# Kernel tuning notes

Measured on AMD Instinct MI355X. Metric: run time of the kernel, lower is better.

Reference implementation:

```python
import jax, jax.numpy as jnp
import numpy as np

B, S, L, H = 64, 256, 4, 1024
S_DIM = 16
LN_EPS = 1e-5
BN_EPS = 1e-5
SM_EPS = 1e-15


def setup_inputs() -> dict:
    key = jax.random.key(0)
    ks = jax.random.split(key, 12)
    inp = {
        'a': jax.random.normal(ks[0], (B, S, L, H), dtype=jnp.float32),
        'b': jax.random.normal(ks[1], (B, S, L, H), dtype=jnp.float32),
        'p': jax.random.normal(ks[2], (B, L, H), dtype=jnp.float32),
        'ap': jax.random.normal(ks[3], (B,), dtype=jnp.float32),
        'bp': jax.random.normal(ks[4], (B,), dtype=jnp.float32),
        # per-layer ffnn: Linear(5H -> S_DIM), stacked over the 4 sim layers
        'ffnn_w': jax.random.normal(ks[5], (L, 5 * H, S_DIM), dtype=jnp.float32) * np.sqrt(2.0 / (5 * H)).astype(np.float32),
        'ffnn_b': jnp.zeros((L, S_DIM), dtype=jnp.float32),
        # BatchNorm1d(S_DIM*L) in eval mode
        'bn_gamma': jnp.ones((S_DIM * L,), dtype=jnp.float32),
        'bn_beta': jnp.zeros((S_DIM * L,), dtype=jnp.float32),
        'bn_rm': jnp.zeros((S_DIM * L,), dtype=jnp.float32),
        'bn_rv': jnp.ones((S_DIM * L,), dtype=jnp.float32),
        # mention_score: Linear(S_DIM*L + 2 -> 3)
        'ms_w': jax.random.normal(ks[6], (S_DIM * L + 2, 3), dtype=jnp.float32) * 0.1,
        'ms_b': jnp.zeros((3,), dtype=jnp.float32),
        # dist_ecoding: Linear(1 -> 1)
        'dist_w': jax.random.normal(ks[7], (), dtype=jnp.float32),
        'dist_b': jnp.zeros((), dtype=jnp.float32),
    }
    return inp


def _layernorm(x):
    m = x.mean(-1, keepdims=True)
    v = jnp.mean((x - m) ** 2, axis=-1, keepdims=True)
    return (x - m) / jnp.sqrt(v + LN_EPS)


def _get_mask(t):
    # 1 up to (exclusive) the first seq position whose [Layer,Feat] slice is all zero
    nonzero = jnp.logical_not(jnp.all(t == 0, axis=(2, 3))).astype(t.dtype)  # [B,S]
    return jnp.cumprod(nonzero, axis=1)


def reference(a, b, p, ap, bp, ffnn_w, ffnn_b, bn_gamma, bn_beta, bn_rm, bn_rv, ms_w, ms_b, dist_w, dist_b):
    rescale = jnp.float32(1.0 / np.sqrt(H))
    a_mask = _get_mask(a)  # [B,S]
    b_mask = _get_mask(b)

    a_ln = _layernorm(a)  # [B,S,L,H]
    b_ln = _layernorm(b)

    # attention scores per layer: [B,L,S]
    sa = jnp.einsum('bslh,blh->bls', a_ln, p) * rescale
    sb = jnp.einsum('bslh,blh->bls', b_ln, p) * rescale

    # masked softmax exactly as in the original (exp * mask / (sum + eps))
    ea = jnp.exp(sa) * a_mask[:, None, :]
    eb = jnp.exp(sb) * b_mask[:, None, :]
    attn_a = ea / (ea.sum(2, keepdims=True) + SM_EPS)
    attn_b = eb / (eb.sum(2, keepdims=True) + SM_EPS)

    pa = jnp.einsum('bls,bslh->blh', attn_a, a_ln)  # pooled a  [B,L,H]
    pb = jnp.einsum('bls,bslh->blh', attn_b, b_ln)

    feat = jnp.concatenate([p, pa, pb, p * pa, p * pb], axis=-1)  # [B,L,5H]
    y = jnp.einsum('blf,lfo->blo', feat, ffnn_w) + ffnn_b  # [B,L,S_DIM]
    y = y.reshape(y.shape[0], -1)  # concat over layers -> [B, L*S_DIM]

    # BatchNorm1d (eval) + ReLU (dropout is identity at inference)
    y = (y - bn_rm) / jnp.sqrt(bn_rv + BN_EPS) * bn_gamma + bn_beta
    y = jax.nn.relu(y)

    ape = jnp.tanh(ap[:, None] * dist_w + dist_b)  # [B,1]
    bpe = jnp.tanh(bp[:, None] * dist_w + dist_b)

    z = jnp.concatenate([y, ape, bpe], axis=1)  # [B, L*S_DIM + 2]
    return z @ ms_w + ms_b  # [B,3]
```

## Files before the change

kernel.cpp:

```cpp
#include <hip/hip_runtime.h>
#include <cstdint>
#include <cstddef>

#define BB_ 64
#define SS_ 256
#define LL_ 4
#define HH_ 1024

#define ZF_OFF   ((size_t)0)
#define MASK_OFF ((size_t)131072)
#define PA_OFF   ((size_t)163840)
#define DEN_OFF  ((size_t)1212416)
#define Y_OFF    ((size_t)1214464)
#define FZ_OFF   ((size_t)1218560)

template <int MODE>
__global__ __launch_bounds__(512) void attn_pool(const float* __restrict__ A_,
                                                 const float* __restrict__ B_,
                                                 const float* __restrict__ P_,
                                                 float* __restrict__ ws) {
  int idx = blockIdx.x;
  int shalf = idx & 1;
  int l = (idx >> 1) & 3;
  int bb = (idx >> 3) & 63;
  int t = idx >> 9;

  if (MODE == 1) {
    const int* fz = reinterpret_cast<const int*>(ws + FZ_OFF);
    if (fz[t * 64 + bb] >= SS_) return;
  }

  const float* __restrict__ X = t ? B_ : A_;
  int tid = threadIdx.x;
  int wid = tid >> 6;
  int ln = tid & 63;

  float pv[16];
  {
    const float4* pr = reinterpret_cast<const float4*>(P_ + ((size_t)bb * LL_ + l) * HH_);
#pragma unroll
    for (int k = 0; k < 4; ++k) {
      float4 v = pr[k * 64 + ln];
      pv[4 * k + 0] = v.x; pv[4 * k + 1] = v.y;
      pv[4 * k + 2] = v.z; pv[4 * k + 3] = v.w;
    }
  }

  float acc[16];
#pragma unroll
  for (int j = 0; j < 16; ++j) acc[j] = 0.f;
  float den = 0.f;

  float* zf = ws + ZF_OFF + (((size_t)t * 64 + bb) * 4 + l) * SS_;
  const float* mk = ws + MASK_OFF + ((size_t)t * 64 + bb) * SS_;

  const float* base = X + (((size_t)bb * SS_ + (size_t)shalf * 128) * LL_ + l) * HH_;

  for (int i = 0; i < 16; ++i) {
    int s_local = i * 8 + wid;
    const float4* row = reinterpret_cast<const float4*>(base + (size_t)s_local * (LL_ * HH_));
    float x[16];
    float s1 = 0.f, s2 = 0.f;
#pragma unroll
    for (int k = 0; k < 4; ++k) {
      float4 v = row[k * 64 + ln];
      x[4 * k + 0] = v.x; x[4 * k + 1] = v.y;
      x[4 * k + 2] = v.z; x[4 * k + 3] = v.w;
      s1 += v.x + v.y + v.z + v.w;
      s2 += v.x * v.x + v.y * v.y + v.z * v.z + v.w * v.w;
    }
#pragma unroll
    for (int off = 32; off > 0; off >>= 1) {
      s1 += __shfl_xor(s1, off);
      s2 += __shfl_xor(s2, off);
    }
    float m = s1 * (1.0f / 1024.0f);
    float var = s2 * (1.0f / 1024.0f) - m * m;
    float rstd = rsqrtf(var + 1e-5f);

    float d = 0.f;
#pragma unroll
    for (int j = 0; j < 16; ++j) {
      x[j] -= m;
      d += x[j] * pv[j];
    }
#pragma unroll
    for (int off = 32; off > 0; off >>= 1) d += __shfl_xor(d, off);

    float e = expf(d * rstd * 0.03125f);
    if (MODE == 0) {
      if (ln == 0) zf[shalf * 128 + s_local] = (s2 == 0.f) ? 1.f : 0.f;
    } else {
      e *= mk[shalf * 128 + s_local];
    }
    float coef = e * rstd;
#pragma unroll
    for (int j = 0; j < 16; ++j) acc[j] += coef * x[j];
    den += e;
  }

  __shared__ float sm[8 * 1024];
#pragma unroll
  for (int k = 0; k < 4; ++k) {
#pragma unroll
    for (int j = 0; j < 4; ++j) sm[wid * 1024 + (k * 64 + ln) * 4 + j] = acc[4 * k + j];
  }
  __syncthreads();
  float* pa = ws + PA_OFF + ((((size_t)shalf * 2 + t) * 64 + bb) * 4 + l) * HH_;
  for (int e2 = tid; e2 < 1024; e2 += 512) {
    float tot = 0.f;
#pragma unroll
    for (int w = 0; w < 8; ++w) tot += sm[w * 1024 + e2];
    pa[e2] = tot;
  }
  __syncthreads();
  if (ln == 0) sm[wid] = den;
  __syncthreads();
  if (tid == 0) {
    float dd = 0.f;
#pragma unroll
    for (int w = 0; w < 8; ++w) dd += sm[w];
    ws[DEN_OFF + (((size_t)shalf * 2 + t) * 64 + bb) * 4 + l] = dd;
  }
}

__global__ __launch_bounds__(256) void mask_kernel(float* __restrict__ ws) {
  int idx = blockIdx.x;
  int t = idx >> 6, bb = idx & 63;
  int s = threadIdx.x;
  const float* zf = ws + ZF_OFF + (((size_t)t * 64 + bb) * 4) * SS_;
  float z0 = zf[0 * SS_ + s], z1 = zf[1 * SS_ + s];
  float z2 = zf[2 * SS_ + s], z3 = zf[3 * SS_ + s];
  bool allzero = (z0 != 0.f) && (z1 != 0.f) && (z2 != 0.f) && (z3 != 0.f);
  int fz = allzero ? s : SS_;
#pragma unroll
  for (int off = 32; off > 0; off >>= 1) fz = min(fz, __shfl_xor(fz, off));
  __shared__ int red[4];
  int wid = s >> 6, ln = s & 63;
  if (ln == 0) red[wid] = fz;
  __syncthreads();
  int fzmin = min(min(red[0], red[1]), min(red[2], red[3]));
  ws[MASK_OFF + ((size_t)t * 64 + bb) * SS_ + s] = (s < fzmin) ? 1.f : 0.f;
  if (s == 0) reinterpret_cast<int*>(ws + FZ_OFF)[t * 64 + bb] = fzmin;
}

__global__ __launch_bounds__(256) void head_kernel(const float* __restrict__ p,
                                                   const float* __restrict__ fw,
                                                   const float* __restrict__ fb,
                                                   float* __restrict__ ws) {
  int blk = blockIdx.x;
  int bb = blk >> 2, l = blk & 3;
  int t = threadIdx.x;

  const float* den = ws + DEN_OFF;
  float inv_a = 1.0f / (den[((0 * 2 + 0) * 64 + bb) * 4 + l] +
                        den[((1 * 2 + 0) * 64 + bb) * 4 + l] + 1e-15f);
  float inv_b = 1.0f / (den[((0 * 2 + 1) * 64 + bb) * 4 + l] +
                        den[((1 * 2 + 1) * 64 + bb) * 4 + l] + 1e-15f);

  const float4* pa00 = reinterpret_cast<const float4*>(ws + PA_OFF + (((size_t)(0 * 2 + 0) * 64 + bb) * 4 + l) * HH_);
  const float4* pa10 = reinterpret_cast<const float4*>(ws + PA_OFF + (((size_t)(1 * 2 + 0) * 64 + bb) * 4 + l) * HH_);
  const float4* pb01 = reinterpret_cast<const float4*>(ws + PA_OFF + (((size_t)(0 * 2 + 1) * 64 + bb) * 4 + l) * HH_);
  const float4* pb11 = reinterpret_cast<const float4*>(ws + PA_OFF + (((size_t)(1 * 2 + 1) * 64 + bb) * 4 + l) * HH_);

  float4 pv = reinterpret_cast<const float4*>(p + ((size_t)bb * LL_ + l) * HH_)[t];
  float4 A0 = pa00[t], A1 = pa10[t], B0 = pb01[t], B1 = pb11[t];
  float av[4] = {(A0.x + A1.x) * inv_a, (A0.y + A1.y) * inv_a,
                 (A0.z + A1.z) * inv_a, (A0.w + A1.w) * inv_a};
  float bv[4] = {(B0.x + B1.x) * inv_b, (B0.y + B1.y) * inv_b,
                 (B0.z + B1.z) * inv_b, (B0.w + B1.w) * inv_b};
  float cp[4] = {pv.x, pv.y, pv.z, pv.w};

  float part[16];
#pragma unroll
  for (int o = 0; o < 16; ++o) part[o] = 0.f;

  const float* wl = fw + (size_t)l * 5120 * 16;
#pragma unroll
  for (int j = 0; j < 4; ++j) {
    int h = t * 4 + j;
    float c[5] = {cp[j], av[j], bv[j], cp[j] * av[j], cp[j] * bv[j]};
#pragma unroll
    for (int sec = 0; sec < 5; ++sec) {
      const float4* wr = reinterpret_cast<const float4*>(wl + ((size_t)sec * 1024 + h) * 16);
#pragma unroll
      for (int o4 = 0; o4 < 4; ++o4) {
        float4 w4 = wr[o4];
        part[o4 * 4 + 0] += c[sec] * w4.x;
        part[o4 * 4 + 1] += c[sec] * w4.y;
        part[o4 * 4 + 2] += c[sec] * w4.z;
        part[o4 * 4 + 3] += c[sec] * w4.w;
      }
    }
  }

  __shared__ float red[256 * 17 + 16 * 17];
#pragma unroll
  for (int o = 0; o < 16; ++o) red[t * 17 + o] = part[o];
  __syncthreads();
  {
    int o = t & 15, g = t >> 4;
    float sacc = 0.f;
#pragma unroll
    for (int i = 0; i < 16; ++i) sacc += red[(g * 16 + i) * 17 + o];
    red[256 * 17 + g * 17 + o] = sacc;
  }
  __syncthreads();
  if (t < 16) {
    float sacc = 0.f;
#pragma unroll
    for (int g = 0; g < 16; ++g) sacc += red[256 * 17 + g * 17 + t];
    ws[Y_OFF + (size_t)bb * 64 + l * 16 + t] = sacc + fb[l * 16 + t];
  }
}

__global__ __launch_bounds__(64) void out_kernel(
    const float* __restrict__ ap, const float* __restrict__ bp,
    const float* __restrict__ gam, const float* __restrict__ bet,
    const float* __restrict__ rm, const float* __restrict__ rv,
    const float* __restrict__ msw, const float* __restrict__ msb,
    const float* __restrict__ dw, const float* __restrict__ db,
    const float* __restrict__ ws, float* __restrict__ out) {
  int bb = blockIdx.x;
  int k = threadIdx.x;
  float yv = ws[Y_OFF + (size_t)bb * 64 + k];
  yv = (yv - rm[k]) * rsqrtf(rv[k] + 1e-5f) * gam[k] + bet[k];
  yv = fmaxf(yv, 0.f);
  float w0 = dw[0], b0 = db[0];
  float ape = tanhf(ap[bb] * w0 + b0);
  float bpe = tanhf(bp[bb] * w0 + b0);
#pragma unroll
  for (int c = 0; c < 3; ++c) {
    float v = yv * msw[k * 3 + c];
#pragma unroll
    for (int off = 32; off > 0; off >>= 1) v += __shfl_xor(v, off);
    if (k == 0) out[bb * 3 + c] = v + ape * msw[64 * 3 + c] + bpe * msw[65 * 3 + c] + msb[c];
  }
}

extern "C" void kernel_launch(void* const* d_in, const int* in_sizes, int n_in,
                              void* d_out, int out_size, void* d_ws, size_t ws_size,
                              hipStream_t stream) {
  (void)in_sizes; (void)n_in; (void)out_size; (void)ws_size;
  const float* a = (const float*)d_in[0];
  const float* b = (const float*)d_in[1];
  const float* p = (const float*)d_in[2];
  const float* ap = (const float*)d_in[3];
  const float* bp = (const float*)d_in[4];
  const float* ffnn_w = (const float*)d_in[5];
  const float* ffnn_b = (const float*)d_in[6];
  const float* bn_g = (const float*)d_in[7];
  const float* bn_b = (const float*)d_in[8];
  const float* bn_rm = (const float*)d_in[9];
  const float* bn_rv = (const float*)d_in[10];
  const float* ms_w = (const float*)d_in[11];
  const float* ms_b = (const float*)d_in[12];
  const float* dist_w = (const float*)d_in[13];
  const float* dist_b = (const float*)d_in[14];
  float* ws = (float*)d_ws;
  float* out = (float*)d_out;

  hipLaunchKernelGGL((attn_pool<0>), dim3(1024), dim3(512), 0, stream, a, b, p, ws);
  hipLaunchKernelGGL(mask_kernel, dim3(128), dim3(256), 0, stream, ws);
  hipLaunchKernelGGL((attn_pool<1>), dim3(1024), dim3(512), 0, stream, a, b, p, ws);
  hipLaunchKernelGGL(head_kernel, dim3(256), dim3(256), 0, stream, p, ffnn_w, ffnn_b, ws);
  hipLaunchKernelGGL(out_kernel, dim3(64), dim3(64), 0, stream,
                     ap, bp, bn_g, bn_b, bn_rm, bn_rv, ms_w, ms_b, dist_w, dist_b, ws, out);
}
```

Before: 129.0 us.

## Fuse mask and head kernels, algebraically fold mean into dot, double-buffer row loads

Folds the mask computation into the second attention pass by having each block recompute the first-zero index from the zero flags, removing a kernel launch and the mask buffer. The score dot product is computed on raw values and corrected by mean times sum(p), and the mean subtraction in the pooled accumulator is deferred to a single correction term. Row loads are software-pipelined two pairs ahead, and p is staged in shared memory. Head and output kernels are merged into one 64-block kernel that loops over layers, which cuts launches but reduces head parallelism from 256 blocks to 64.

```diff
diff --git a/kernel.cpp b/kernel.cpp
--- a/kernel.cpp
+++ b/kernel.cpp
@@ -2,104 +2,168 @@
 #include <cstdint>
 #include <cstddef>
 
-#define BB_ 64
 #define SS_ 256
 #define LL_ 4
 #define HH_ 1024
 
 #define ZF_OFF   ((size_t)0)
-#define MASK_OFF ((size_t)131072)
-#define PA_OFF   ((size_t)163840)
-#define DEN_OFF  ((size_t)1212416)
-#define Y_OFF    ((size_t)1214464)
-#define FZ_OFF   ((size_t)1218560)
+#define PA_OFF   ((size_t)131072)
+#define DEN_OFF  ((size_t)(131072 + 1048576))
 
 template <int MODE>
-__global__ __launch_bounds__(512) void attn_pool(const float* __restrict__ A_,
-                                                 const float* __restrict__ B_,
-                                                 const float* __restrict__ P_,
-                                                 float* __restrict__ ws) {
+__global__ __launch_bounds__(512, 4) void attn_pool(const float* __restrict__ A_,
+                                                    const float* __restrict__ B_,
+                                                    const float* __restrict__ P_,
+                                                    float* __restrict__ ws) {
   int idx = blockIdx.x;
   int shalf = idx & 1;
   int l = (idx >> 1) & 3;
   int bb = (idx >> 3) & 63;
   int t = idx >> 9;
-
-  if (MODE == 1) {
-    const int* fz = reinterpret_cast<const int*>(ws + FZ_OFF);
-    if (fz[t * 64 + bb] >= SS_) return;
-  }
-
-  const float* __restrict__ X = t ? B_ : A_;
   int tid = threadIdx.x;
   int wid = tid >> 6;
   int ln = tid & 63;
 
-  float pv[16];
+  __shared__ float pshare[1024];
+  __shared__ float sm[8 * 1024];
+  __shared__ int wmin[8];
+
+  int fz = SS_;
+  if (MODE == 1) {
+    int myfz = SS_;
+    if (tid < SS_) {
+      const float* zfb = ws + ZF_OFF + ((size_t)t * 64 + bb) * 4 * SS_;
+      bool az = (zfb[0 * SS_ + tid] != 0.f) && (zfb[1 * SS_ + tid] != 0.f) &&
+                (zfb[2 * SS_ + tid] != 0.f) && (zfb[3 * SS_ + tid] != 0.f);
+      myfz = az ? tid : SS_;
+    }
+#pragma unroll
+    for (int off = 32; off > 0; off >>= 1) myfz = min(myfz, __shfl_xor(myfz, off));
+    if (ln == 0) wmin[wid] = myfz;
+    __syncthreads();
+#pragma unroll
+    for (int w = 0; w < 8; ++w) fz = min(fz, wmin[w]);
+    if (fz >= SS_) return;
+    __syncthreads();
+  }
+
+  const float* __restrict__ X = t ? B_ : A_;
+
+  if (tid < 256) {
+    reinterpret_cast<float4*>(pshare)[tid] =
+        reinterpret_cast<const float4*>(P_ + ((size_t)bb * LL_ + l) * HH_)[tid];
+  }
+  __syncthreads();
+
+  float sump = 0.f;
   {
-    const float4* pr = reinterpret_cast<const float4*>(P_ + ((size_t)bb * LL_ + l) * HH_);
+    const float4 pw0 = *reinterpret_cast<const float4*>(&pshare[(0 * 64 + ln) * 4]);
+    const float4 pw1 = *reinterpret_cast<const float4*>(&pshare[(1 * 64 + ln) * 4]);
+    const float4 pw2 = *reinterpret_cast<const float4*>(&pshare[(2 * 64 + ln) * 4]);
+    const float4 pw3 = *reinterpret_cast<const float4*>(&pshare[(3 * 64 + ln) * 4]);
+    sump = (pw0.x + pw0.y + pw0.z + pw0.w) + (pw1.x + pw1.y + pw1.z + pw1.w) +
+           (pw2.x + pw2.y + pw2.z + pw2.w) + (pw3.x + pw3.y + pw3.z + pw3.w);
+#pragma unroll
+    for (int off = 32; off > 0; off >>= 1) sump += __shfl_xor(sump, off);
+  }
+
+  const float* base = X + (((size_t)bb * SS_ + (size_t)shalf * 128) * LL_ + l) * HH_;
+  float* zfp = ws + ZF_OFF + (((size_t)t * 64 + bb) * 4 + l) * SS_;
+
+  float acc[16];
+#pragma unroll
+  for (int j = 0; j < 16; ++j) acc[j] = 0.f;
+  float den = 0.f, cm = 0.f;
+
+  auto loadRow = [&](float (&dst)[16], int sl) {
+    const float4* rp = reinterpret_cast<const float4*>(base + (size_t)sl * (LL_ * HH_));
+    float4 v0 = rp[ln], v1 = rp[64 + ln], v2 = rp[128 + ln], v3 = rp[192 + ln];
+    dst[0] = v0.x;  dst[1] = v0.y;  dst[2] = v0.z;  dst[3] = v0.w;
+    dst[4] = v1.x;  dst[5] = v1.y;  dst[6] = v1.z;  dst[7] = v1.w;
+    dst[8] = v2.x;  dst[9] = v2.y;  dst[10] = v2.z; dst[11] = v2.w;
+    dst[12] = v3.x; dst[13] = v3.y; dst[14] = v3.z; dst[15] = v3.w;
+  };
+
+  auto processPair = [&](const float (&u)[16], const float (&v)[16], int slu, int slv) {
+    float a1 = 0.f, a2 = 0.f, a3 = 0.f, b1 = 0.f, b2 = 0.f, b3 = 0.f;
 #pragma unroll
     for (int k = 0; k < 4; ++k) {
-      float4 v = pr[k * 64 + ln];
-      pv[4 * k + 0] = v.x; pv[4 * k + 1] = v.y;
-      pv[4 * k + 2] = v.z; pv[4 * k + 3] = v.w;
-    }
-  }
-
-  float acc[16];
-#pragma unroll
-  for (int j = 0; j < 16; ++j) acc[j] = 0.f;
-  float den = 0.f;
-
-  float* zf = ws + ZF_OFF + (((size_t)t * 64 + bb) * 4 + l) * SS_;
-  const float* mk = ws + MASK_OFF + ((size_t)t * 64 + bb) * SS_;
-
-  const float* base = X + (((size_t)bb * SS_ + (size_t)shalf * 128) * LL_ + l) * HH_;
-
-  for (int i = 0; i < 16; ++i) {
-    int s_local = i * 8 + wid;
-    const float4* row = reinterpret_cast<const float4*>(base + (size_t)s_local * (LL_ * HH_));
-    float x[16];
-    float s1 = 0.f, s2 = 0.f;
-#pragma unroll
-    for (int k = 0; k < 4; ++k) {
-      float4 v = row[k * 64 + ln];
-      x[4 * k + 0] = v.x; x[4 * k + 1] = v.y;
-      x[4 * k + 2] = v.z; x[4 * k + 3] = v.w;
-      s1 += v.x + v.y + v.z + v.w;
-      s2 += v.x * v.x + v.y * v.y + v.z * v.z + v.w * v.w;
+      const float4 pw = *reinterpret_cast<const float4*>(&pshare[(k * 64 + ln) * 4]);
+      a1 += u[4 * k + 0] + u[4 * k + 1] + u[4 * k + 2] + u[4 * k + 3];
+      a2 = fmaf(u[4 * k + 0], u[4 * k + 0], fmaf(u[4 * k + 1], u[4 * k + 1],
+           fmaf(u[4 * k + 2], u[4 * k + 2], fmaf(u[4 * k + 3], u[4 * k + 3], a2))));
+      a3 = fmaf(u[4 * k + 0], pw.x, fmaf(u[4 * k + 1], pw.y,
+           fmaf(u[4 * k + 2], pw.z, fmaf(u[4 * k + 3], pw.w, a3))));
+      b1 += v[4 * k + 0] + v[4 * k + 1] + v[4 * k + 2] + v[4 * k + 3];
+      b2 = fmaf(v[4 * k + 0], v[4 * k + 0], fmaf(v[4 * k + 1], v[4 * k + 1],
+           fmaf(v[4 * k + 2], v[4 * k + 2], fmaf(v[4 * k + 3], v[4 * k + 3], b2))));
+      b3 = fmaf(v[4 * k + 0], pw.x, fmaf(v[4 * k + 1], pw.y,
+           fmaf(v[4 * k + 2], pw.z, fmaf(v[4 * k + 3], pw.w, b3))));
     }
 #pragma unroll
     for (int off = 32; off > 0; off >>= 1) {
-      s1 += __shfl_xor(s1, off);
-      s2 += __shfl_xor(s2, off);
-    }
-    float m = s1 * (1.0f / 1024.0f);
-    float var = s2 * (1.0f / 1024.0f) - m * m;
-    float rstd = rsqrtf(var + 1e-5f);
-
-    float d = 0.f;
-#pragma unroll
-    for (int j = 0; j < 16; ++j) {
-      x[j] -= m;
-      d += x[j] * pv[j];
-    }
-#pragma unroll
-    for (int off = 32; off > 0; off >>= 1) d += __shfl_xor(d, off);
-
-    float e = expf(d * rstd * 0.03125f);
-    if (MODE == 0) {
-      if (ln == 0) zf[shalf * 128 + s_local] = (s2 == 0.f) ? 1.f : 0.f;
-    } else {
-      e *= mk[shalf * 128 + s_local];
-    }
-    float coef = e * rstd;
-#pragma unroll
-    for (int j = 0; j < 16; ++j) acc[j] += coef * x[j];
-    den += e;
-  }
-
-  __shared__ float sm[8 * 1024];
+      a1 += __shfl_xor(a1, off); a2 += __shfl_xor(a2, off); a3 += __shfl_xor(a3, off);
+      b1 += __shfl_xor(b1, off); b2 += __shfl_xor(b2, off); b3 += __shfl_xor(b3, off);
+    }
+    {
+      float m_ = a1 * (1.f / 1024.f);
+      float var_ = fmaf(-m_, m_, a2 * (1.f / 1024.f));
+      float rstd_ = rsqrtf(var_ + 1e-5f);
+      float d_ = (a3 - m_ * sump) * rstd_ * 0.03125f;
+      float e_ = expf(d_);
+      int sg_ = shalf * 128 + slu;
+      if (MODE == 0) {
+        if (ln == 0) zfp[sg_] = (a2 == 0.f) ? 1.f : 0.f;
+      } else {
+        if (sg_ >= fz) e_ = 0.f;
+      }
+      float coef_ = e_ * rstd_;
+#pragma unroll
+      for (int j = 0; j < 16; ++j) acc[j] = fmaf(coef_, u[j], acc[j]);
+      cm = fmaf(coef_, m_, cm);
+      den += e_;
+    }
+    {
+      float m_ = b1 * (1.f / 1024.f);
+      float var_ = fmaf(-m_, m_, b2 * (1.f / 1024.f));
+      float rstd_ = rsqrtf(var_ + 1e-5f);
+      float d_ = (b3 - m_ * sump) * rstd_ * 0.03125f;
+      float e_ = expf(d_);
+      int sg_ = shalf * 128 + slv;
+      if (MODE == 0) {
+        if (ln == 0) zfp[sg_] = (b2 == 0.f) ? 1.f : 0.f;
+      } else {
+        if (sg_ >= fz) e_ = 0.f;
+      }
+      float coef_ = e_ * rstd_;
+#pragma unroll
+      for (int j = 0; j < 16; ++j) acc[j] = fmaf(coef_, v[j], acc[j]);
+      cm = fmaf(coef_, m_, cm);
+      den += e_;
+    }
+  };
+
+  float xa[16], xb[16], ya[16], yb[16];
+  loadRow(xa, wid + 0);   loadRow(xb, wid + 8);
+  loadRow(ya, wid + 16);  loadRow(yb, wid + 24);
+  processPair(xa, xb, wid + 0, wid + 8);
+  loadRow(xa, wid + 32);  loadRow(xb, wid + 40);
+  processPair(ya, yb, wid + 16, wid + 24);
+  loadRow(ya, wid + 48);  loadRow(yb, wid + 56);
+  processPair(xa, xb, wid + 32, wid + 40);
+  loadRow(xa, wid + 64);  loadRow(xb, wid + 72);
+  processPair(ya, yb, wid + 48, wid + 56);
+  loadRow(ya, wid + 80);  loadRow(yb, wid + 88);
+  processPair(xa, xb, wid + 64, wid + 72);
+  loadRow(xa, wid + 96);  loadRow(xb, wid + 104);
+  processPair(ya, yb, wid + 80, wid + 88);
+  loadRow(ya, wid + 112); loadRow(yb, wid + 120);
+  processPair(xa, xb, wid + 96, wid + 104);
+  processPair(ya, yb, wid + 112, wid + 120);
+
+#pragma unroll
+  for (int j = 0; j < 16; ++j) acc[j] -= cm;
+
 #pragma unroll
   for (int k = 0; k < 4; ++k) {
 #pragma unroll
@@ -124,97 +188,8 @@
   }
 }
 
-__global__ __launch_bounds__(256) void mask_kernel(float* __restrict__ ws) {
-  int idx = blockIdx.x;
-  int t = idx >> 6, bb = idx & 63;
-  int s = threadIdx.x;
-  const float* zf = ws + ZF_OFF + (((size_t)t * 64 + bb) * 4) * SS_;
-  float z0 = zf[0 * SS_ + s], z1 = zf[1 * SS_ + s];
-  float z2 = zf[2 * SS_ + s], z3 = zf[3 * SS_ + s];
-  bool allzero = (z0 != 0.f) && (z1 != 0.f) && (z2 != 0.f) && (z3 != 0.f);
-  int fz = allzero ? s : SS_;
-#pragma unroll
-  for (int off = 32; off > 0; off >>= 1) fz = min(fz, __shfl_xor(fz, off));
-  __shared__ int red[4];
-  int wid = s >> 6, ln = s & 63;
-  if (ln == 0) red[wid] = fz;
-  __syncthreads();
-  int fzmin = min(min(red[0], red[1]), min(red[2], red[3]));
-  ws[MASK_OFF + ((size_t)t * 64 + bb) * SS_ + s] = (s < fzmin) ? 1.f : 0.f;
-  if (s == 0) reinterpret_cast<int*>(ws + FZ_OFF)[t * 64 + bb] = fzmin;
-}
-
-__global__ __launch_bounds__(256) void head_kernel(const float* __restrict__ p,
-                                                   const float* __restrict__ fw,
-                                                   const float* __restrict__ fb,
-                                                   float* __restrict__ ws) {
-  int blk = blockIdx.x;
-  int bb = blk >> 2, l = blk & 3;
-  int t = threadIdx.x;
-
-  const float* den = ws + DEN_OFF;
-  float inv_a = 1.0f / (den[((0 * 2 + 0) * 64 + bb) * 4 + l] +
-                        den[((1 * 2 + 0) * 64 + bb) * 4 + l] + 1e-15f);
-  float inv_b = 1.0f / (den[((0 * 2 + 1) * 64 + bb) * 4 + l] +
-                        den[((1 * 2 + 1) * 64 + bb) * 4 + l] + 1e-15f);
-
-  const float4* pa00 = reinterpret_cast<const float4*>(ws + PA_OFF + (((size_t)(0 * 2 + 0) * 64 + bb) * 4 + l) * HH_);
-  const float4* pa10 = reinterpret_cast<const float4*>(ws + PA_OFF + (((size_t)(1 * 2 + 0) * 64 + bb) * 4 + l) * HH_);
-  const float4* pb01 = reinterpret_cast<const float4*>(ws + PA_OFF + (((size_t)(0 * 2 + 1) * 64 + bb) * 4 + l) * HH_);
-  const float4* pb11 = reinterpret_cast<const float4*>(ws + PA_OFF + (((size_t)(1 * 2 + 1) * 64 + bb) * 4 + l) * HH_);
-
-  float4 pv = reinterpret_cast<const float4*>(p + ((size_t)bb * LL_ + l) * HH_)[t];
-  float4 A0 = pa00[t], A1 = pa10[t], B0 = pb01[t], B1 = pb11[t];
-  float av[4] = {(A0.x + A1.x) * inv_a, (A0.y + A1.y) * inv_a,
-                 (A0.z + A1.z) * inv_a, (A0.w + A1.w) * inv_a};
-  float bv[4] = {(B0.x + B1.x) * inv_b, (B0.y + B1.y) * inv_b,
-                 (B0.z + B1.z) * inv_b, (B0.w + B1.w) * inv_b};
-  float cp[4] = {pv.x, pv.y, pv.z, pv.w};
-
-  float part[16];
-#pragma unroll
-  for (int o = 0; o < 16; ++o) part[o] = 0.f;
-
-  const float* wl = fw + (size_t)l * 5120 * 16;
-#pragma unroll
-  for (int j = 0; j < 4; ++j) {
-    int h = t * 4 + j;
-    float c[5] = {cp[j], av[j], bv[j], cp[j] * av[j], cp[j] * bv[j]};
-#pragma unroll
-    for (int sec = 0; sec < 5; ++sec) {
-      const float4* wr = reinterpret_cast<const float4*>(wl + ((size_t)sec * 1024 + h) * 16);
-#pragma unroll
-      for (int o4 = 0; o4 < 4; ++o4) {
-        float4 w4 = wr[o4];
-        part[o4 * 4 + 0] += c[sec] * w4.x;
-        part[o4 * 4 + 1] += c[sec] * w4.y;
-        part[o4 * 4 + 2] += c[sec] * w4.z;
-        part[o4 * 4 + 3] += c[sec] * w4.w;
-      }
-    }
-  }
-
-  __shared__ float red[256 * 17 + 16 * 17];
-#pragma unroll
-  for (int o = 0; o < 16; ++o) red[t * 17 + o] = part[o];
-  __syncthreads();
-  {
-    int o = t & 15, g = t >> 4;
-    float sacc = 0.f;
-#pragma unroll
-    for (int i = 0; i < 16; ++i) sacc += red[(g * 16 + i) * 17 + o];
-    red[256 * 17 + g * 17 + o] = sacc;
-  }
-  __syncthreads();
-  if (t < 16) {
-    float sacc = 0.f;
-#pragma unroll
-    for (int g = 0; g < 16; ++g) sacc += red[256 * 17 + g * 17 + t];
-    ws[Y_OFF + (size_t)bb * 64 + l * 16 + t] = sacc + fb[l * 16 + t];
-  }
-}
-
-__global__ __launch_bounds__(64) void out_kernel(
+__global__ __launch_bounds__(256) void headout_kernel(
+    const float* __restrict__ p, const float* __restrict__ fw, const float* __restrict__ fb,
     const float* __restrict__ ap, const float* __restrict__ bp,
     const float* __restrict__ gam, const float* __restrict__ bet,
     const float* __restrict__ rm, const float* __restrict__ rv,
@@ -222,19 +197,88 @@
     const float* __restrict__ dw, const float* __restrict__ db,
     const float* __restrict__ ws, float* __restrict__ out) {
   int bb = blockIdx.x;
-  int k = threadIdx.x;
-  float yv = ws[Y_OFF + (size_t)bb * 64 + k];
-  yv = (yv - rm[k]) * rsqrtf(rv[k] + 1e-5f) * gam[k] + bet[k];
-  yv = fmaxf(yv, 0.f);
-  float w0 = dw[0], b0 = db[0];
-  float ape = tanhf(ap[bb] * w0 + b0);
-  float bpe = tanhf(bp[bb] * w0 + b0);
-#pragma unroll
-  for (int c = 0; c < 3; ++c) {
-    float v = yv * msw[k * 3 + c];
-#pragma unroll
-    for (int off = 32; off > 0; off >>= 1) v += __shfl_xor(v, off);
-    if (k == 0) out[bb * 3 + c] = v + ape * msw[64 * 3 + c] + bpe * msw[65 * 3 + c] + msb[c];
+  int t = threadIdx.x;
+  __shared__ float red[256 * 17 + 16 * 17];
+  __shared__ float yv[64];
+  const float* den = ws + DEN_OFF;
+
+  for (int l = 0; l < 4; ++l) {
+    float inv_a = 1.0f / (den[((0 * 2 + 0) * 64 + bb) * 4 + l] +
+                          den[((1 * 2 + 0) * 64 + bb) * 4 + l] + 1e-15f);
+    float inv_b = 1.0f / (den[((0 * 2 + 1) * 64 + bb) * 4 + l] +
+                          den[((1 * 2 + 1) * 64 + bb) * 4 + l] + 1e-15f);
+
+    const float4* pa00 = reinterpret_cast<const float4*>(ws + PA_OFF + (((size_t)(0 * 2 + 0) * 64 + bb) * 4 + l) * HH_);
+    const float4* pa10 = reinterpret_cast<const float4*>(ws + PA_OFF + (((size_t)(1 * 2 + 0) * 64 + bb) * 4 + l) * HH_);
+    const float4* pb01 = reinterpret_cast<const float4*>(ws + PA_OFF + (((size_t)(0 * 2 + 1) * 64 + bb) * 4 + l) * HH_);
+    const float4* pb11 = reinterpret_cast<const float4*>(ws + PA_OFF + (((size_t)(1 * 2 + 1) * 64 + bb) * 4 + l) * HH_);
+
+    float4 pv = reinterpret_cast<const float4*>(p + ((size_t)bb * LL_ + l) * HH_)[t];
+    float4 A0 = pa00[t], A1 = pa10[t], B0 = pb01[t], B1 = pb11[t];
+    float av[4] = {(A0.x + A1.x) * inv_a, (A0.y + A1.y) * inv_a,
+                   (A0.z + A1.z) * inv_a, (A0.w + A1.w) * inv_a};
+    float bv[4] = {(B0.x + B1.x) * inv_b, (B0.y + B1.y) * inv_b,
+                   (B0.z + B1.z) * inv_b, (B0.w + B1.w) * inv_b};
+    float cp[4] = {pv.x, pv.y, pv.z, pv.w};
+
+    float part[16];
+#pragma unroll
+    for (int o = 0; o < 16; ++o) part[o] = 0.f;
+
+    const float* wl = fw + (size_t)l * 5120 * 16;
+#pragma unroll
+    for (int j = 0; j < 4; ++j) {
+      int h = t * 4 + j;
+      float c[5] = {cp[j], av[j], bv[j], cp[j] * av[j], cp[j] * bv[j]};
+#pragma unroll
+      for (int sec = 0; sec < 5; ++sec) {
+        const float4* wr = reinterpret_cast<const float4*>(wl + ((size_t)sec * 1024 + h) * 16);
+#pragma unroll
+        for (int o4 = 0; o4 < 4; ++o4) {
+          float4 w4 = wr[o4];
+          part[o4 * 4 + 0] += c[sec] * w4.x;
+          part[o4 * 4 + 1] += c[sec] * w4.y;
+          part[o4 * 4 + 2] += c[sec] * w4.z;
+          part[o4 * 4 + 3] += c[sec] * w4.w;
+        }
+      }
+    }
+
+#pragma unroll
+    for (int o = 0; o < 16; ++o) red[t * 17 + o] = part[o];
+    __syncthreads();
+    {
+      int o = t & 15, g = t >> 4;
+      float sacc = 0.f;
+#pragma unroll
+      for (int i = 0; i < 16; ++i) sacc += red[(g * 16 + i) * 17 + o];
+      red[256 * 17 + g * 17 + o] = sacc;
+    }
+    __syncthreads();
+    if (t < 16) {
+      float sacc = 0.f;
+#pragma unroll
+      for (int g = 0; g < 16; ++g) sacc += red[256 * 17 + g * 17 + t];
+      yv[l * 16 + t] = sacc + fb[l * 16 + t];
+    }
+    __syncthreads();
+  }
+
+  if (t < 64) {
+    int k = t;
+    float y = yv[k];
+    y = (y - rm[k]) * rsqrtf(rv[k] + 1e-5f) * gam[k] + bet[k];
+    y = fmaxf(y, 0.f);
+    float w0 = dw[0], b0 = db[0];
+    float ape = tanhf(ap[bb] * w0 + b0);
+    float bpe = tanhf(bp[bb] * w0 + b0);
+#pragma unroll
+    for (int c = 0; c < 3; ++c) {
+      float v = y * msw[k * 3 + c];
+#pragma unroll
+      for (int off = 32; off > 0; off >>= 1) v += __shfl_xor(v, off);
+      if (k == 0) out[bb * 3 + c] = v + ape * msw[64 * 3 + c] + bpe * msw[65 * 3 + c] + msb[c];
+    }
   }
 }
 
@@ -261,9 +305,8 @@
   float* out = (float*)d_out;
 
   hipLaunchKernelGGL((attn_pool<0>), dim3(1024), dim3(512), 0, stream, a, b, p, ws);
-  hipLaunchKernelGGL(mask_kernel, dim3(128), dim3(256), 0, stream, ws);
   hipLaunchKernelGGL((attn_pool<1>), dim3(1024), dim3(512), 0, stream, a, b, p, ws);
-  hipLaunchKernelGGL(head_kernel, dim3(256), dim3(256), 0, stream, p, ffnn_w, ffnn_b, ws);
-  hipLaunchKernelGGL(out_kernel, dim3(64), dim3(64), 0, stream,
-                     ap, bp, bn_g, bn_b, bn_rm, bn_rv, ms_w, ms_b, dist_w, dist_b, ws, out);
+  hipLaunchKernelGGL(headout_kernel, dim3(64), dim3(256), 0, stream,
+                     p, ffnn_w, ffnn_b, ap, bp, bn_g, bn_b, bn_rm, bn_rv,
+                     ms_w, ms_b, dist_w, dist_b, ws, out);
 }
```

Result: slower. 393.5 us (+205.1%).
